# Performance work log

Hardware: AMD Instinct MI355X
Metric: run time of the kernel (lower is better)

Reference implementation:

```python
import jax, jax.numpy as jnp
import numpy as np

N_USERS = 100000
N_ITEMS = 50000
N_NODES = N_USERS + N_ITEMS
DIM = 64
N_HOPS = 3
NNZ = 3200000
BATCH = 4096
K = 4
DECAY = 1e-4


def setup_inputs() -> dict:
    key = jax.random.key(0)
    ks = jax.random.split(key, 8)
    user_embed = jax.random.normal(ks[0], (N_USERS, DIM), dtype=jnp.float32) * 0.1
    item_embed = jax.random.normal(ks[1], (N_ITEMS, DIM), dtype=jnp.float32) * 0.1
    adj_rows = jax.random.randint(ks[2], (NNZ,), 0, N_NODES, dtype=jnp.int32)
    adj_cols = jax.random.randint(ks[3], (NNZ,), 0, N_NODES, dtype=jnp.int32)
    # normalized-adjacency-like small positive values
    adj_vals = jax.random.uniform(ks[4], (NNZ,), dtype=jnp.float32) * 0.05
    users = jax.random.randint(ks[5], (BATCH,), 0, N_USERS, dtype=jnp.int32)
    pos_items = jax.random.randint(ks[6], (BATCH,), 0, N_ITEMS, dtype=jnp.int32)
    neg_items = jax.random.randint(ks[7], (BATCH, K), 0, N_ITEMS, dtype=jnp.int32)
    return {"user_embed": user_embed, "item_embed": item_embed,
            "adj_vals": adj_vals, "adj_rows": adj_rows, "adj_cols": adj_cols,
            "users": users, "pos_items": pos_items, "neg_items": neg_items}


def _gcn(user_embed, item_embed, adj_vals, adj_rows, adj_cols):
    """LightGCN propagation: n_hops of SpMM, stack per-hop embeddings."""
    all_embed = jnp.concatenate([user_embed, item_embed], axis=0)  # [N, d]
    agg = all_embed
    embs = [all_embed]
    for _ in range(N_HOPS):
        msg = adj_vals[:, None] * agg[adj_cols]                    # [nnz, d]
        agg = jax.ops.segment_sum(msg, adj_rows, num_segments=N_NODES)
        embs.append(agg)
    embs = jnp.stack(embs, axis=1)                                 # [N, hops+1, d]
    return embs[:N_USERS], embs[N_USERS:]


def reference(user_embed, item_embed, adj_vals, adj_rows, adj_cols,
              users, pos_items, neg_items):
    user_gcn, item_gcn = _gcn(user_embed, item_embed, adj_vals, adj_rows, adj_cols)
    u_g = user_gcn[users]            # [B, hops+1, d]
    p_g = item_gcn[pos_items]        # [B, hops+1, d]
    n_g = item_gcn[neg_items]        # [B, K, hops+1, d]
    # pooling == 'mean' over hop axis
    u_e = u_g.mean(axis=1)
    pos_e = p_g.mean(axis=1)
    neg_e = n_g.mean(axis=2)         # [B, K, d]
    pos_scores = jnp.sum(u_e * pos_e, axis=-1)                     # [B]
    neg_scores = jnp.sum(u_e[:, None, :] * neg_e, axis=-1)         # [B, K]
    # BCE with logits: labels 1 for pos, 0 for neg
    pos_loss = jax.nn.softplus(-pos_scores)
    neg_loss = jax.nn.softplus(neg_scores).sum(axis=1)
    mf_loss = pos_loss + neg_loss
    regularize = (jnp.sum(u_g[:, 0, :] ** 2)
                  + jnp.sum(p_g[:, 0, :] ** 2)
                  + jnp.sum(n_g[:, :, 0, :] ** 2)) / 2.0
    emb_loss = DECAY * regularize / BATCH
    return mf_loss.mean() + emb_loss
```

## Files before the change

kernel.cpp:

```cpp
#include <hip/hip_runtime.h>
#include <hip/hip_bf16.h>
#include <math.h>

#define N_USERS 100000
#define N_ITEMS 50000
#define N_NODES 150000
#define DIM     64
#define N_HOPS  3
#define NNZ     3200000
#define BATCH   4096
#define KNEG    4
#define DECAY   1e-4f
#define BATCH_TOT (BATCH * (2 + KNEG))

#define NBUCK   586
#define NCHUNK  512
#define CHUNK   (NNZ / NCHUNK)
#define CAP     8192
#define BH_N    (NBUCK * NCHUNK)
#define S1_N    ((BH_N + 255) / 256)
#define S2_N    ((S1_N + 255) / 256)

typedef unsigned short ushort_t;
typedef unsigned int uint_t;
typedef unsigned long long u64_t;
typedef float v2f __attribute__((ext_vector_type(2)));

#if __has_builtin(__builtin_amdgcn_cvt_pk_f32_fp8) && __has_builtin(__builtin_amdgcn_cvt_pk_fp8_f32)
#define HAVE_FP8_CVT 1
#else
#define HAVE_FP8_CVT 0
#endif

#if !HAVE_FP8_CVT
__device__ __forceinline__ float dec1_(uint_t b) {
    uint_t s = b >> 7, e = (b >> 3) & 15, m = b & 7;
    float mag = e ? __uint_as_float(((e + 120u) << 23) | (m << 20))
                  : (float)m * 0.001953125f;
    return s ? -mag : mag;
}
__device__ __forceinline__ uint_t enc1_(float x) {
    float ax = fabsf(x);
    uint_t s = (__float_as_uint(x) >> 31) << 7;
    if (!(ax > 0.f)) return s;
    if (ax >= 448.f) return s | 0x7E;
    if (ax < 0.015625f) {
        int m = (int)rintf(ax * 512.0f);
        if (m >= 8) return s | 0x08;
        return s | (uint_t)m;
    }
    uint_t u = __float_as_uint(ax);
    u += 0x7FFFF + ((u >> 20) & 1);
    int e = (int)((u >> 23) & 0xFF) - 127 + 7;
    if (e >= 16) return s | 0x7E;
    if (e <= 0)  return s | 0x08;
    return s | ((uint_t)e << 3) | ((u >> 20) & 7);
}
#endif

__device__ __forceinline__ void dec4(uint_t u, float* f) {
#if HAVE_FP8_CVT
    v2f lo = __builtin_amdgcn_cvt_pk_f32_fp8(u, false);
    v2f hi = __builtin_amdgcn_cvt_pk_f32_fp8(u, true);
    f[0] = lo[0]; f[1] = lo[1]; f[2] = hi[0]; f[3] = hi[1];
#else
    f[0] = dec1_(u & 255); f[1] = dec1_((u >> 8) & 255);
    f[2] = dec1_((u >> 16) & 255); f[3] = dec1_(u >> 24);
#endif
}

__device__ __forceinline__ uint_t enc4(const float* f) {
#if HAVE_FP8_CVT
    int t = __builtin_amdgcn_cvt_pk_fp8_f32(f[0], f[1], 0, false);
    t = __builtin_amdgcn_cvt_pk_fp8_f32(f[2], f[3], t, true);
    return (uint_t)t;
#else
    return enc1_(f[0]) | (enc1_(f[1]) << 8) | (enc1_(f[2]) << 16) | (enc1_(f[3]) << 24);
#endif
}


__global__ __launch_bounds__(512) void k_scatter(
        const int* __restrict__ rows, const int* __restrict__ cols,
        const float* __restrict__ vals, int* __restrict__ bh,
        int* __restrict__ sloc, u64_t* __restrict__ ebuf) {
    __shared__ u64_t stage[CHUNK];
    __shared__ int hist[NBUCK];
    __shared__ int cursor[NBUCK];
    __shared__ int part[512];
    int t = threadIdx.x, b = blockIdx.x;
    for (int i = t; i < NBUCK; i += 512) hist[i] = 0;
    __syncthreads();
    int base0 = b * CHUNK;
    for (int e = base0 + t; e < base0 + CHUNK; e += 512)
        atomicAdd(&hist[rows[e] >> 8], 1);
    __syncthreads();
    for (int i = t; i < NBUCK; i += 512)
        bh[(size_t)i * NCHUNK + b] = hist[i];
    int a0 = (2 * t     < NBUCK) ? hist[2 * t]     : 0;
    int a1 = (2 * t + 1 < NBUCK) ? hist[2 * t + 1] : 0;
    part[t] = a0 + a1;
    __syncthreads();
    for (int o = 1; o < 512; o <<= 1) {
        int x = (t >= o) ? part[t - o] : 0;
        __syncthreads();
        part[t] += x;
        __syncthreads();
    }
    int ebase = part[t] - (a0 + a1);
    __syncthreads();
    if (2 * t < NBUCK)     hist[2 * t] = ebase;
    if (2 * t + 1 < NBUCK) hist[2 * t + 1] = ebase + a0;
    __syncthreads();
    for (int i = t; i < NBUCK; i += 512) {
        sloc[(size_t)b * NBUCK + i] = hist[i];
        cursor[i] = hist[i];
    }
    __syncthreads();
    for (int e = base0 + t; e < base0 + CHUNK; e += 512) {
        int r = rows[e];
        int slot = atomicAdd(&cursor[r >> 8], 1);
        stage[slot] = ((u64_t)(uint_t)__float_as_int(vals[e]) << 32)
                    | ((u64_t)(r & 255) << 18) | (u64_t)cols[e];
    }
    __syncthreads();
    for (int i = t; i < CHUNK; i += 512)
        ebuf[base0 + i] = stage[i];
}

__global__ void k_scanA(int* __restrict__ data, int* __restrict__ bsums, int n) {
    __shared__ int lds[256];
    int t = threadIdx.x;
    int i = blockIdx.x * 256 + t;
    int v = (i < n) ? data[i] : 0;
    lds[t] = v; __syncthreads();
    for (int o = 1; o < 256; o <<= 1) {
        int x = (t >= o) ? lds[t - o] : 0;
        __syncthreads();
        lds[t] += x;
        __syncthreads();
    }
    if (i < n) data[i] = lds[t] - v;
    if (t == 255) bsums[blockIdx.x] = lds[t];
}

__global__ void k_scan_small(int* __restrict__ data, int n) {
    __shared__ int lds[1024];
    int t = threadIdx.x;
    int v = (t < n) ? data[t] : 0;
    lds[t] = v; __syncthreads();
    for (int o = 1; o < 1024; o <<= 1) {
        int x = (t >= o) ? lds[t - o] : 0;
        __syncthreads();
        lds[t] += x;
        __syncthreads();
    }
    if (t < n) data[t] = lds[t] - v;
}

__global__ void k_addback(int* __restrict__ data, const int* __restrict__ offs, int n) {
    int i = blockIdx.x * blockDim.x + threadIdx.x;
    if (i < n) data[i] += offs[i >> 8];
}

__global__ void k_bucket_csr(const u64_t* __restrict__ ebuf, const int* __restrict__ bh,
                             const int* __restrict__ sloc,
                             int2* __restrict__ edges, int* __restrict__ row_ptr) {
    __shared__ u64_t stage[CAP];
    __shared__ int hist[256];
    __shared__ int sbuf[256];
    int t = threadIdx.x, b = blockIdx.x;
    int S = bh[(size_t)b * NCHUNK];
    int E = (b + 1 < NBUCK) ? bh[(size_t)(b + 1) * NCHUNK] : NNZ;
    int cnt = E - S;
    if (cnt > CAP) cnt = CAP;
    hist[t] = 0;
    __syncthreads();
    int wid = t >> 6, lane = t & 63;
    int sub = lane >> 3, j0 = lane & 7;
    for (int c = wid * 8; c < NCHUNK; c += 32) {
        int bch = c + sub;
        int lo = sloc[(size_t)bch * NBUCK + b];
        int hi = (b + 1 < NBUCK) ? sloc[(size_t)bch * NBUCK + b + 1] : CHUNK;
        int dst = bh[(size_t)b * NCHUNK + bch] - S;
        for (int j = j0; j < hi - lo; j += 8) {
            if (dst + j < CAP)
                stage[dst + j] = ebuf[(size_t)bch * CHUNK + lo + j];
        }
    }
    __syncthreads();
    for (int i = t; i < cnt; i += 256)
        atomicAdd(&hist[(int)((stage[i] >> 18) & 255)], 1);
    __syncthreads();
    int v = hist[t];
    sbuf[t] = v; __syncthreads();
    for (int o = 1; o < 256; o <<= 1) {
        int x = (t >= o) ? sbuf[t - o] : 0;
        __syncthreads();
        sbuf[t] += x;
        __syncthreads();
    }
    int excl = sbuf[t] - v;
    int grow = (b << 8) + t;
    if (grow < N_NODES) row_ptr[grow] = S + excl;
    if (b == 0 && t == 0) row_ptr[N_NODES] = NNZ;
    hist[t] = excl;
    __syncthreads();
    for (int i = t; i < cnt; i += 256) {
        u64_t pk = stage[i];
        int rl = (int)((pk >> 18) & 255);
        int slot = atomicAdd(&hist[rl], 1);
        edges[S + slot] = make_int2((int)(pk & 0x3FFFF), (int)(pk >> 32));
    }
}


__global__ void k_tofp8(const float* __restrict__ ue, const float* __restrict__ ie,
                        uint2* __restrict__ outq) {
    int idx = blockIdx.x * blockDim.x + threadIdx.x;
    const int total8 = N_NODES * DIM / 8;
    if (idx >= total8) return;
    const int u8 = N_USERS * DIM / 8;
    const float4* src = (idx < u8) ? (const float4*)ue + 2 * (size_t)idx
                                   : (const float4*)ie + 2 * (size_t)(idx - u8);
    float4 a = src[0], b = src[1];
    float fa[4] = {a.x, a.y, a.z, a.w};
    float fb[4] = {b.x, b.y, b.z, b.w};
    outq[idx] = make_uint2(enc4(fa), enc4(fb));
}

__device__ __forceinline__ void fma8(uint2 r, float v, float* acc) {
    float f[4];
    dec4(r.x, f);
    acc[0] += v * f[0]; acc[1] += v * f[1]; acc[2] += v * f[2]; acc[3] += v * f[3];
    dec4(r.y, f);
    acc[4] += v * f[0]; acc[5] += v * f[1]; acc[6] += v * f[2]; acc[7] += v * f[3];
}

__device__ __forceinline__ void row_accum8(const uint2* __restrict__ srcq,
                                           const int2* __restrict__ edges,
                                           int s, int e, int oct, int ol,
                                           float* acc) {
    int i = s;
    for (; i + 16 <= e; i += 16) {
        int2 e0 = edges[i + oct];
        int2 e1 = edges[i + 8 + oct];
        uint2 r0 = srcq[(size_t)e0.x * 8 + ol];
        uint2 r1 = srcq[(size_t)e1.x * 8 + ol];
        fma8(r0, __int_as_float(e0.y), acc);
        fma8(r1, __int_as_float(e1.y), acc);
    }
    for (; i + 8 <= e; i += 8) {
        int2 ed = edges[i + oct];
        uint2 r = srcq[(size_t)ed.x * 8 + ol];
        fma8(r, __int_as_float(ed.y), acc);
    }
    int rem = e - i;
    if (oct < rem) {
        int2 ed = edges[i + oct];
        uint2 r = srcq[(size_t)ed.x * 8 + ol];
        fma8(r, __int_as_float(ed.y), acc);
    }
}

__device__ __forceinline__ void oct_reduce(float* acc) {
    #pragma unroll
    for (int j = 0; j < 8; ++j) {
        acc[j] += __shfl_xor(acc[j], 8);
        acc[j] += __shfl_xor(acc[j], 16);
        acc[j] += __shfl_xor(acc[j], 32);
    }
}

__global__ void k_spmm(const uint2* __restrict__ srcq, uint2* __restrict__ outq,
                       const int* __restrict__ row_ptr, const int2* __restrict__ edges) {
    int w = (blockIdx.x * blockDim.x + threadIdx.x) >> 6;
    int lane = threadIdx.x & 63;
    if (w >= N_NODES) return;
    int oct = lane >> 3, ol = lane & 7;
    int s = row_ptr[w], e = row_ptr[w + 1];
    float acc[8] = {0.f, 0.f, 0.f, 0.f, 0.f, 0.f, 0.f, 0.f};
    row_accum8(srcq, edges, s, e, oct, ol, acc);
    oct_reduce(acc);
    if (oct == 0)
        outq[(size_t)w * 8 + ol] = make_uint2(enc4(acc), enc4(acc + 4));
}

__device__ __forceinline__ void batch_map(int w, const int* __restrict__ users,
                                          const int* __restrict__ pos, const int* __restrict__ neg,
                                          float* u_acc, float* p_acc, float* n_acc,
                                          int& node, float*& dst) {
    if (w < BATCH)            { node = users[w];                        dst = u_acc + (size_t)w * DIM; }
    else if (w < 2 * BATCH)   { int j = w - BATCH;     node = N_USERS + pos[j]; dst = p_acc + (size_t)j * DIM; }
    else                      { int j = w - 2 * BATCH; node = N_USERS + neg[j]; dst = n_acc + (size_t)j * DIM; }
}

template<int INIT>
__global__ void k_gather_accum(const uint_t* __restrict__ src,
                               const int* __restrict__ users, const int* __restrict__ pos,
                               const int* __restrict__ neg,
                               float* __restrict__ u_acc, float* __restrict__ p_acc,
                               float* __restrict__ n_acc) {
    int gid = blockIdx.x * blockDim.x + threadIdx.x;
    int w4 = gid >> 6;
    int lane = threadIdx.x & 63;
    int slot = w4 * 4 + (lane >> 4);
    int dquad = lane & 15;
    if (slot >= BATCH_TOT) return;
    int node; float* dst;
    batch_map(slot, users, pos, neg, u_acc, p_acc, n_acc, node, dst);
    float f[4];
    dec4(src[(size_t)node * 16 + dquad], f);
    float4* d4 = (float4*)(dst + 4 * dquad);
    if (INIT) {
        *d4 = make_float4(f[0], f[1], f[2], f[3]);
    } else {
        float4 cur = *d4;
        cur.x += f[0]; cur.y += f[1]; cur.z += f[2]; cur.w += f[3];
        *d4 = cur;
    }
}

__global__ void k_spmm_batch(const uint2* __restrict__ srcq,
                             const int* __restrict__ row_ptr, const int2* __restrict__ edges,
                             const int* __restrict__ users, const int* __restrict__ pos,
                             const int* __restrict__ neg,
                             float* __restrict__ u_acc, float* __restrict__ p_acc,
                             float* __restrict__ n_acc) {
    int w = (blockIdx.x * blockDim.x + threadIdx.x) >> 6;
    int lane = threadIdx.x & 63;
    if (w >= BATCH_TOT) return;
    int oct = lane >> 3, ol = lane & 7;
    int node; float* dst;
    batch_map(w, users, pos, neg, u_acc, p_acc, n_acc, node, dst);
    int s = row_ptr[node], e = row_ptr[node + 1];
    float acc[8] = {0.f, 0.f, 0.f, 0.f, 0.f, 0.f, 0.f, 0.f};
    row_accum8(srcq, edges, s, e, oct, ol, acc);
    oct_reduce(acc);
    if (oct == 0) {
        #pragma unroll
        for (int j = 0; j < 8; ++j) dst[8 * ol + j] += acc[j];
    }
}

__global__ void k_zero_out(float* out) { out[0] = 0.f; }

__device__ __forceinline__ float softplus(float x) {
    return log1pf(expf(-fabsf(x))) + fmaxf(x, 0.f);
}

__device__ __forceinline__ float wave_sum(float v) {
    for (int o = 32; o > 0; o >>= 1) v += __shfl_xor(v, o);
    return v;
}

__global__ void k_loss(const float* __restrict__ u_acc, const float* __restrict__ p_acc,
                       const float* __restrict__ n_acc,
                       const float* __restrict__ ue, const float* __restrict__ ie,
                       const int* __restrict__ users, const int* __restrict__ pos,
                       const int* __restrict__ neg, float* __restrict__ out) {
    int w = (blockIdx.x * blockDim.x + threadIdx.x) >> 6;
    int lane = threadIdx.x & 63;
    if (w >= BATCH) return;
    const float inv = 1.0f / (N_HOPS + 1);
    float u0 = ue[(size_t)users[w] * DIM + lane];
    float p0 = ie[(size_t)pos[w]  * DIM + lane];
    float u = (u_acc[(size_t)w * DIM + lane] + u0) * inv;
    float p = (p_acc[(size_t)w * DIM + lane] + p0) * inv;
    float pos_score = wave_sum(u * p);
    float loss = softplus(-pos_score);
    float r = u0 * u0 + p0 * p0;
    #pragma unroll
    for (int k = 0; k < KNEG; ++k) {
        float n0 = ie[(size_t)neg[w * KNEG + k] * DIM + lane];
        float nk = (n_acc[((size_t)w * KNEG + k) * DIM + lane] + n0) * inv;
        float neg_score = wave_sum(u * nk);
        loss += softplus(neg_score);
        r += n0 * n0;
    }
    r = wave_sum(r);
    float contrib = loss * (1.0f / BATCH) + (DECAY * 0.5f / BATCH) * r;
    if (lane == 0) atomicAdd(out, contrib);
}


extern "C" void kernel_launch(void* const* d_in, const int* in_sizes, int n_in,
                              void* d_out, int out_size, void* d_ws, size_t ws_size,
                              hipStream_t stream) {
    const float* user_embed = (const float*)d_in[0];
    const float* item_embed = (const float*)d_in[1];
    const float* adj_vals   = (const float*)d_in[2];
    const int*   adj_rows   = (const int*)d_in[3];
    const int*   adj_cols   = (const int*)d_in[4];
    const int*   users      = (const int*)d_in[5];
    const int*   pos_items  = (const int*)d_in[6];
    const int*   neg_items  = (const int*)d_in[7];
    float* out = (float*)d_out;

    int2* edges   = (int2*)d_ws;
    u64_t* ebuf   = (u64_t*)(edges + NNZ);
    float* u_acc  = (float*)(ebuf + NNZ);
    float* p_acc  = u_acc + (size_t)BATCH * DIM;
    float* n_acc  = p_acc + (size_t)BATCH * DIM;
    uint2* bufB   = (uint2*)(n_acc + (size_t)BATCH * KNEG * DIM);
    uint2* buf1   = bufB + (size_t)N_NODES * 8;
    int* row_ptr  = (int*)(buf1 + (size_t)N_NODES * 8);
    int* bh       = row_ptr + N_NODES + 1;
    int* S1       = bh + BH_N;
    int* S2       = S1 + S1_N;
    int* sloc     = S2 + S2_N + 11;
    uint2* buf0   = (uint2*)ebuf;

    const int T = 256;

    k_scatter<<<NCHUNK, 512, 0, stream>>>(adj_rows, adj_cols, adj_vals, bh, sloc, ebuf);
    k_scanA<<<S1_N, 256, 0, stream>>>(bh, S1, BH_N);
    k_scanA<<<S2_N, 256, 0, stream>>>(S1, S2, S1_N);
    k_scan_small<<<1, 1024, 0, stream>>>(S2, S2_N);
    k_addback<<<(S1_N + T - 1) / T, T, 0, stream>>>(S1, S2, S1_N);
    k_addback<<<(BH_N + T - 1) / T, T, 0, stream>>>(bh, S1, BH_N);
    k_bucket_csr<<<NBUCK, 256, 0, stream>>>(ebuf, bh, sloc, edges, row_ptr);

    k_tofp8<<<(N_NODES * DIM / 8 + T - 1) / T, T, 0, stream>>>(user_embed, item_embed, bufB);

    int sb = (N_NODES * 64 + T - 1) / T;
    int gb = (BATCH_TOT * 64 + T - 1) / T;
    int gb4 = ((BATCH_TOT / 4) * 64 + T - 1) / T;

    k_spmm<<<sb, T, 0, stream>>>(bufB, buf0, row_ptr, edges);
    k_gather_accum<1><<<gb4, T, 0, stream>>>((const uint_t*)buf0, users, pos_items, neg_items,
                                             u_acc, p_acc, n_acc);
    k_spmm<<<sb, T, 0, stream>>>(buf0, buf1, row_ptr, edges);
    k_gather_accum<0><<<gb4, T, 0, stream>>>((const uint_t*)buf1, users, pos_items, neg_items,
                                             u_acc, p_acc, n_acc);
    k_spmm_batch<<<gb, T, 0, stream>>>(buf1, row_ptr, edges,
                                       users, pos_items, neg_items,
                                       u_acc, p_acc, n_acc);

    k_zero_out<<<1, 1, 0, stream>>>(out);
    k_loss<<<(BATCH * 64 + T - 1) / T, T, 0, stream>>>(
        u_acc, p_acc, n_acc, user_embed, item_embed, users, pos_items, neg_items, out);
}
```

Baseline: 307.0 us.

## Transpose bucket histograms coalescedly, single-pass mid scan, batch first SpMM gathers

k_scatter now writes its per-chunk bucket counts and local offsets contiguously by chunk instead of strided by bucket. A tiled LDS transpose kernel then converts both arrays to bucket-major layout, so the global stores and bucket_csr's sloc reads are coalesced. The three-kernel second-level scan is replaced by one 1024-thread kernel that scans 2048 entries. Separately, row_accum8 now issues up to four edge loads and their gathers before the FMAs, adding memory-level parallelism for short rows at the cost of extra registers.

```diff
diff --git a/kernel.cpp b/kernel.cpp
--- a/kernel.cpp
+++ b/kernel.cpp
@@ -19,7 +19,6 @@
 #define CAP     8192
 #define BH_N    (NBUCK * NCHUNK)
 #define S1_N    ((BH_N + 255) / 256)
-#define S2_N    ((S1_N + 255) / 256)
 
 typedef unsigned short ushort_t;
 typedef unsigned int uint_t;
@@ -82,8 +81,8 @@
 
 __global__ __launch_bounds__(512) void k_scatter(
         const int* __restrict__ rows, const int* __restrict__ cols,
-        const float* __restrict__ vals, int* __restrict__ bh,
-        int* __restrict__ sloc, u64_t* __restrict__ ebuf) {
+        const float* __restrict__ vals, int* __restrict__ bhc,
+        int* __restrict__ sloc_c, u64_t* __restrict__ ebuf) {
     __shared__ u64_t stage[CHUNK];
     __shared__ int hist[NBUCK];
     __shared__ int cursor[NBUCK];
@@ -96,7 +95,7 @@
         atomicAdd(&hist[rows[e] >> 8], 1);
     __syncthreads();
     for (int i = t; i < NBUCK; i += 512)
-        bh[(size_t)i * NCHUNK + b] = hist[i];
+        bhc[(size_t)b * NBUCK + i] = hist[i];
     int a0 = (2 * t     < NBUCK) ? hist[2 * t]     : 0;
     int a1 = (2 * t + 1 < NBUCK) ? hist[2 * t + 1] : 0;
     part[t] = a0 + a1;
@@ -113,7 +112,7 @@
     if (2 * t + 1 < NBUCK) hist[2 * t + 1] = ebase + a0;
     __syncthreads();
     for (int i = t; i < NBUCK; i += 512) {
-        sloc[(size_t)b * NBUCK + i] = hist[i];
+        sloc_c[(size_t)b * NBUCK + i] = hist[i];
         cursor[i] = hist[i];
     }
     __syncthreads();
@@ -126,6 +125,25 @@
     __syncthreads();
     for (int i = t; i < CHUNK; i += 512)
         ebuf[base0 + i] = stage[i];
+}
+
+__global__ void k_transpose(const int* __restrict__ inA, int* __restrict__ outA,
+                            const int* __restrict__ inB, int* __restrict__ outB) {
+    __shared__ int tile[32][33];
+    const int* in = blockIdx.z ? inB : inA;
+    int* out      = blockIdx.z ? outB : outA;
+    int bx = blockIdx.x * 32;
+    int by = blockIdx.y * 32;
+    int tx = threadIdx.x, ty = threadIdx.y;
+    for (int r = ty; r < 32; r += 8) {
+        int c = by + r, k = bx + tx;
+        tile[r][tx] = (k < NBUCK) ? in[(size_t)c * NBUCK + k] : 0;
+    }
+    __syncthreads();
+    for (int r = ty; r < 32; r += 8) {
+        int k = bx + r, c = by + tx;
+        if (k < NBUCK) out[(size_t)k * NCHUNK + c] = tile[tx][r];
+    }
 }
 
 __global__ void k_scanA(int* __restrict__ data, int* __restrict__ bsums, int n) {
@@ -144,18 +162,22 @@
     if (t == 255) bsums[blockIdx.x] = lds[t];
 }
 
-__global__ void k_scan_small(int* __restrict__ data, int n) {
-    __shared__ int lds[1024];
+__global__ void k_scan2048(int* __restrict__ data, int n) {
+    __shared__ int part[1024];
     int t = threadIdx.x;
-    int v = (t < n) ? data[t] : 0;
-    lds[t] = v; __syncthreads();
+    int a0 = (2 * t     < n) ? data[2 * t]     : 0;
+    int a1 = (2 * t + 1 < n) ? data[2 * t + 1] : 0;
+    part[t] = a0 + a1;
+    __syncthreads();
     for (int o = 1; o < 1024; o <<= 1) {
-        int x = (t >= o) ? lds[t - o] : 0;
-        __syncthreads();
-        lds[t] += x;
-        __syncthreads();
-    }
-    if (t < n) data[t] = lds[t] - v;
+        int x = (t >= o) ? part[t - o] : 0;
+        __syncthreads();
+        part[t] += x;
+        __syncthreads();
+    }
+    int base = part[t] - (a0 + a1);
+    if (2 * t < n)     data[2 * t] = base;
+    if (2 * t + 1 < n) data[2 * t + 1] = base + a0;
 }
 
 __global__ void k_addback(int* __restrict__ data, const int* __restrict__ offs, int n) {
@@ -164,7 +186,7 @@
 }
 
 __global__ void k_bucket_csr(const u64_t* __restrict__ ebuf, const int* __restrict__ bh,
-                             const int* __restrict__ sloc,
+                             const int* __restrict__ sloc_t,
                              int2* __restrict__ edges, int* __restrict__ row_ptr) {
     __shared__ u64_t stage[CAP];
     __shared__ int hist[256];
@@ -180,8 +202,8 @@
     int sub = lane >> 3, j0 = lane & 7;
     for (int c = wid * 8; c < NCHUNK; c += 32) {
         int bch = c + sub;
-        int lo = sloc[(size_t)bch * NBUCK + b];
-        int hi = (b + 1 < NBUCK) ? sloc[(size_t)bch * NBUCK + b + 1] : CHUNK;
+        int lo = sloc_t[(size_t)b * NCHUNK + bch];
+        int hi = (b + 1 < NBUCK) ? sloc_t[(size_t)(b + 1) * NCHUNK + bch] : CHUNK;
         int dst = bh[(size_t)b * NCHUNK + bch] - S;
         for (int j = j0; j < hi - lo; j += 8) {
             if (dst + j < CAP)
@@ -241,7 +263,22 @@
                                            const int2* __restrict__ edges,
                                            int s, int e, int oct, int ol,
                                            float* acc) {
-    int i = s;
+    int len = e - s;
+    if (len <= 0) return;
+    int ng = (len + 7) >> 3; if (ng > 4) ng = 4;
+    int2 ed[4]; uint2 rr[4];
+    #pragma unroll
+    for (int g = 0; g < 4; ++g) {
+        int idx = s + 8 * g + oct;
+        ed[g] = (g < ng && idx < e) ? edges[idx] : make_int2(0, 0);
+    }
+    #pragma unroll
+    for (int g = 0; g < 4; ++g)
+        rr[g] = srcq[(size_t)ed[g].x * 8 + ol];
+    #pragma unroll
+    for (int g = 0; g < 4; ++g)
+        fma8(rr[g], __int_as_float(ed[g].y), acc);
+    int i = s + 8 * ng;
     for (; i + 16 <= e; i += 16) {
         int2 e0 = edges[i + oct];
         int2 e1 = edges[i + 8 + oct];
@@ -251,15 +288,15 @@
         fma8(r1, __int_as_float(e1.y), acc);
     }
     for (; i + 8 <= e; i += 8) {
-        int2 ed = edges[i + oct];
-        uint2 r = srcq[(size_t)ed.x * 8 + ol];
-        fma8(r, __int_as_float(ed.y), acc);
+        int2 ed1 = edges[i + oct];
+        uint2 r = srcq[(size_t)ed1.x * 8 + ol];
+        fma8(r, __int_as_float(ed1.y), acc);
     }
     int rem = e - i;
     if (oct < rem) {
-        int2 ed = edges[i + oct];
-        uint2 r = srcq[(size_t)ed.x * 8 + ol];
-        fma8(r, __int_as_float(ed.y), acc);
+        int2 ed1 = edges[i + oct];
+        uint2 r = srcq[(size_t)ed1.x * 8 + ol];
+        fma8(r, __int_as_float(ed1.y), acc);
     }
 }
 
@@ -406,20 +443,23 @@
     uint2* buf1   = bufB + (size_t)N_NODES * 8;
     int* row_ptr  = (int*)(buf1 + (size_t)N_NODES * 8);
     int* bh       = row_ptr + N_NODES + 1;
-    int* S1       = bh + BH_N;
-    int* S2       = S1 + S1_N;
-    int* sloc     = S2 + S2_N + 11;
+    int* bhc      = bh + BH_N;
+    int* sloc_t   = bhc + BH_N;
+    int* sloc_c   = sloc_t + BH_N;
+    int* S1       = sloc_c + BH_N;
     uint2* buf0   = (uint2*)ebuf;
 
     const int T = 256;
 
-    k_scatter<<<NCHUNK, 512, 0, stream>>>(adj_rows, adj_cols, adj_vals, bh, sloc, ebuf);
+    k_scatter<<<NCHUNK, 512, 0, stream>>>(adj_rows, adj_cols, adj_vals, bhc, sloc_c, ebuf);
+    {
+        dim3 g((NBUCK + 31) / 32, NCHUNK / 32, 2), b(32, 8);
+        k_transpose<<<g, b, 0, stream>>>(bhc, bh, sloc_c, sloc_t);
+    }
     k_scanA<<<S1_N, 256, 0, stream>>>(bh, S1, BH_N);
-    k_scanA<<<S2_N, 256, 0, stream>>>(S1, S2, S1_N);
-    k_scan_small<<<1, 1024, 0, stream>>>(S2, S2_N);
-    k_addback<<<(S1_N + T - 1) / T, T, 0, stream>>>(S1, S2, S1_N);
+    k_scan2048<<<1, 1024, 0, stream>>>(S1, S1_N);
     k_addback<<<(BH_N + T - 1) / T, T, 0, stream>>>(bh, S1, BH_N);
-    k_bucket_csr<<<NBUCK, 256, 0, stream>>>(ebuf, bh, sloc, edges, row_ptr);
+    k_bucket_csr<<<NBUCK, 256, 0, stream>>>(ebuf, bh, sloc_t, edges, row_ptr);
 
     k_tofp8<<<(N_NODES * DIM / 8 + T - 1) / T, T, 0, stream>>>(user_embed, item_embed, bufB);
 
```

New measurement: 309.1 us. About the same (+0.7%).
